# Optimization experiments

Hardware: AMD Instinct MI355X
Metric: run time of the kernel (lower is better)

Reference implementation:

```python
import jax, jax.numpy as jnp
import numpy as np

B, N = 8192, 2048


def setup_inputs() -> dict:
    key = jax.random.key(0)
    k1, k2 = jax.random.split(key)
    predictions = jax.random.normal(k1, (B, N), dtype=jnp.float32)
    targets = jax.random.normal(k2, (B, N), dtype=jnp.float32)
    return {"predictions": predictions, "targets": targets}


def reference(predictions, targets):
    # Original: per-batch NxN squared-difference cost matrix + scipy Hungarian,
    # then MSE(pred, optimally-permuted targets), averaged over the batch.
    # For scalar entries with cost (p_i - t_j)^2 the optimal assignment is the
    # monotone matching (rearrangement inequality): sort both vectors and pair
    # in order. This computes the exact same loss, fully vectorized.
    p_sorted = jnp.sort(predictions, axis=-1)  # [B, N]
    t_sorted = jnp.sort(targets, axis=-1)      # [B, N]
    # mean over N per row, then mean over B == global mean
    return jnp.mean((p_sorted - t_sorted) ** 2)
```

## Files before the change

### kernel.cpp

```cpp
#include <hip/hip_runtime.h>
#include <math.h>

#define ROWS 8192
#define NCOL 2048
#define V 32
#define WPB 4
#define THREADS (WPB * 64)

#define DPP_XOR1 0xB1
#define DPP_XOR2 0x4E
#define DPP_XOR3 0x1B
#define DPP_XOR7 0x141
#define DPP_XOR15 0x140

__device__ __forceinline__ void ce(float& a, float& b) {
  const float lo = fminf(a, b);
  const float hi = fmaxf(a, b);
  a = lo; b = hi;
}

__device__ __forceinline__ float ce_dir(float a, float b, float cdir) {
  return __builtin_amdgcn_fmed3f(a, b, cdir);
}

__device__ __forceinline__ float dirc(int lane, int bit) {
  return (lane & bit) ? INFINITY : -INFINITY;
}

template <int CTRL>
__device__ __forceinline__ float dpp_x(float x) {
  return __int_as_float(__builtin_amdgcn_update_dpp(
      0, __float_as_int(x), CTRL, 0xF, 0xF, true));
}

__device__ __forceinline__ float bperm(int addr, float x) {
  return __int_as_float(__builtin_amdgcn_ds_bpermute(addr, __float_as_int(x)));
}

template <int CTRL>
__device__ __forceinline__ void dpp_xor_pass(float r[V], float cdir) {
#pragma unroll
  for (int v = 0; v < V; ++v) r[v] = ce_dir(r[v], dpp_x<CTRL>(r[v]), cdir);
}

template <int CTRL>
__device__ __forceinline__ void dpp_flip_pass(float r[V], float cdir) {
#pragma unroll
  for (int q = 0; q < 8; ++q) {
    const int vA = 2 * q, vB = 2 * q + 1;
    float o[4];
    o[0] = dpp_x<CTRL>(r[vA ^ 31]);
    o[1] = dpp_x<CTRL>(r[vB ^ 31]);
    o[2] = dpp_x<CTRL>(r[vB]);
    o[3] = dpp_x<CTRL>(r[vA]);
    r[vA]      = ce_dir(r[vA],      o[0], cdir);
    r[vB]      = ce_dir(r[vB],      o[1], cdir);
    r[vB ^ 31] = ce_dir(r[vB ^ 31], o[2], cdir);
    r[vA ^ 31] = ce_dir(r[vA ^ 31], o[3], cdir);
  }
}

__device__ __forceinline__ void ds_xor_pass(float r[V], int addr, float cdir) {
#pragma unroll
  for (int c = 0; c < V; c += 8) {
    float o[8];
#pragma unroll
    for (int u = 0; u < 8; ++u) o[u] = bperm(addr, r[c + u]);
#pragma unroll
    for (int u = 0; u < 8; ++u) r[c + u] = ce_dir(r[c + u], o[u], cdir);
  }
}

__device__ __forceinline__ void ds_flip_pass(float r[V], int addr, float cdir) {
#pragma unroll
  for (int q = 0; q < 8; ++q) {
    const int vA = 2 * q, vB = 2 * q + 1;
    float o[4];
    o[0] = bperm(addr, r[vA ^ 31]);
    o[1] = bperm(addr, r[vB ^ 31]);
    o[2] = bperm(addr, r[vB]);
    o[3] = bperm(addr, r[vA]);
    r[vA]      = ce_dir(r[vA],      o[0], cdir);
    r[vB]      = ce_dir(r[vB],      o[1], cdir);
    r[vB ^ 31] = ce_dir(r[vB ^ 31], o[2], cdir);
    r[vA ^ 31] = ce_dir(r[vA ^ 31], o[3], cdir);
  }
}

__device__ __forceinline__ void inlane_tail(float rp[V], float rt[V]) {
#pragma unroll
  for (int j = 16; j >= 1; j >>= 1) {
#pragma unroll
    for (int v = 0; v < V; ++v) {
      if ((v & j) == 0) {
        ce(rp[v], rp[v | j]);
        ce(rt[v], rt[v | j]);
      }
    }
  }
}

__global__ __launch_bounds__(THREADS, 3) void sort_mse_kernel(
    const float* __restrict__ pred, const float* __restrict__ targ,
    float* __restrict__ out) {
  const int lane = threadIdx.x & 63;
  const int wave = threadIdx.x >> 6;
  const int row = blockIdx.x * WPB + wave;
  const size_t base = (size_t)row * NCOL + (size_t)lane * V;

  float rp[V], rt[V];
  const float4* p4 = (const float4*)(pred + base);
  const float4* t4 = (const float4*)(targ + base);
#pragma unroll
  for (int q = 0; q < V / 4; ++q) {
    const float4 a = p4[q];
    rp[4 * q + 0] = a.x; rp[4 * q + 1] = a.y;
    rp[4 * q + 2] = a.z; rp[4 * q + 3] = a.w;
    const float4 b = t4[q];
    rt[4 * q + 0] = b.x; rt[4 * q + 1] = b.y;
    rt[4 * q + 2] = b.z; rt[4 * q + 3] = b.w;
  }

#pragma unroll
  for (int k = 2; k <= V; k <<= 1) {
#pragma unroll
    for (int v = 0; v < V; ++v) {
      if ((v & (k >> 1)) == 0) {
        ce(rp[v], rp[v ^ (k - 1)]);
        ce(rt[v], rt[v ^ (k - 1)]);
      }
    }
#pragma unroll
    for (int j = k >> 2; j >= 1; j >>= 1) {
#pragma unroll
      for (int v = 0; v < V; ++v) {
        if ((v & j) == 0) {
          ce(rp[v], rp[v | j]);
          ce(rt[v], rt[v | j]);
        }
      }
    }
  }

#pragma unroll 1
  for (int kb = 1; kb <= 32; kb <<= 1) {
    const float cf = dirc(lane, kb);
    if (kb == 1) {
      dpp_flip_pass<DPP_XOR1>(rp, cf);  dpp_flip_pass<DPP_XOR1>(rt, cf);
    } else if (kb == 2) {
      dpp_flip_pass<DPP_XOR3>(rp, cf);  dpp_flip_pass<DPP_XOR3>(rt, cf);
    } else if (kb == 4) {
      dpp_flip_pass<DPP_XOR7>(rp, cf);  dpp_flip_pass<DPP_XOR7>(rt, cf);
    } else if (kb == 8) {
      dpp_flip_pass<DPP_XOR15>(rp, cf); dpp_flip_pass<DPP_XOR15>(rt, cf);
    } else {
      const int a = ((lane ^ (2 * kb - 1)) << 2);
      ds_flip_pass(rp, a, cf); ds_flip_pass(rt, a, cf);
    }
#pragma unroll 1
    for (int m = kb >> 1; m >= 1; m >>= 1) {
      const float c = dirc(lane, m);
      if (m == 1) {
        dpp_xor_pass<DPP_XOR1>(rp, c); dpp_xor_pass<DPP_XOR1>(rt, c);
      } else if (m == 2) {
        dpp_xor_pass<DPP_XOR2>(rp, c); dpp_xor_pass<DPP_XOR2>(rt, c);
      } else {
        const int a = ((lane ^ m) << 2);
        ds_xor_pass(rp, a, c); ds_xor_pass(rt, a, c);
      }
    }
    inlane_tail(rp, rt);
  }

  float acc = 0.f;
#pragma unroll
  for (int v = 0; v < V; ++v) {
    const float d = rp[v] - rt[v];
    acc = fmaf(d, d, acc);
  }
#pragma unroll
  for (int off = 32; off > 0; off >>= 1) acc += __shfl_down(acc, off, 64);
  if (lane == 0) {
    unsafeAtomicAdd(out, acc * (1.0f / ((float)ROWS * (float)NCOL)));
  }
}

extern "C" void kernel_launch(void* const* d_in, const int* in_sizes, int n_in,
                              void* d_out, int out_size, void* d_ws, size_t ws_size,
                              hipStream_t stream) {
  const float* pred = (const float*)d_in[0];
  const float* targ = (const float*)d_in[1];
  float* out = (float*)d_out;

  hipMemsetAsync(out, 0, sizeof(float), stream);
  sort_mse_kernel<<<ROWS / WPB, THREADS, 0, stream>>>(pred, targ, out);
}
```

Measured before the change: 248.7 us.

## Sort predictions and targets sequentially, stash sorted predictions in LDS, use DPP for xor4/xor8

Instead of sorting both rows together in registers, the kernel sorts the prediction row, parks it in swizzled shared memory, then sorts the target row and compares against the stash. This halves register pressure, so launch bounds go from 3 to 4 waves per SIMD. It also replaces the ds_bpermute exchanges for xor distances 4 and 8 with DPP shifts and row_xmask. The cost is lost ILP from no longer interleaving two independent sorts, plus an LDS round trip.

```diff
diff --git a/kernel.cpp b/kernel.cpp
--- a/kernel.cpp
+++ b/kernel.cpp
@@ -7,11 +7,14 @@
 #define WPB 4
 #define THREADS (WPB * 64)
 
-#define DPP_XOR1 0xB1
-#define DPP_XOR2 0x4E
-#define DPP_XOR3 0x1B
-#define DPP_XOR7 0x141
+#define DPP_XOR1  0xB1
+#define DPP_XOR2  0x4E
+#define DPP_XOR3  0x1B
+#define DPP_XOR7  0x141
 #define DPP_XOR15 0x140
+#define DPP_XOR8  0x128
+#define DPP_SHL4  0x104
+#define DPP_SHR4  0x114
 
 __device__ __forceinline__ void ce(float& a, float& b) {
   const float lo = fminf(a, b);
@@ -41,6 +44,16 @@
 __device__ __forceinline__ void dpp_xor_pass(float r[V], float cdir) {
 #pragma unroll
   for (int v = 0; v < V; ++v) r[v] = ce_dir(r[v], dpp_x<CTRL>(r[v]), cdir);
+}
+
+__device__ __forceinline__ void dpp_xor4_pass(float r[V], float cdir, int lane) {
+  const bool hi = (lane & 4) != 0;
+#pragma unroll
+  for (int v = 0; v < V; ++v) {
+    const float a = dpp_x<DPP_SHL4>(r[v]);
+    const float b = dpp_x<DPP_SHR4>(r[v]);
+    r[v] = ce_dir(r[v], hi ? b : a, cdir);
+  }
 }
 
 template <int CTRL>
@@ -87,96 +100,85 @@
   }
 }
 
-__device__ __forceinline__ void inlane_tail(float rp[V], float rt[V]) {
+__device__ __forceinline__ void sort_row(float r[V], const int lane) {
 #pragma unroll
-  for (int j = 16; j >= 1; j >>= 1) {
+  for (int k = 2; k <= V; k <<= 1) {
 #pragma unroll
-    for (int v = 0; v < V; ++v) {
-      if ((v & j) == 0) {
-        ce(rp[v], rp[v | j]);
-        ce(rt[v], rt[v | j]);
-      }
+    for (int v = 0; v < V; ++v)
+      if ((v & (k >> 1)) == 0) ce(r[v], r[v ^ (k - 1)]);
+#pragma unroll
+    for (int j = k >> 2; j >= 1; j >>= 1)
+#pragma unroll
+      for (int v = 0; v < V; ++v)
+        if ((v & j) == 0) ce(r[v], r[v | j]);
+  }
+#pragma unroll 1
+  for (int kb = 1; kb <= 32; kb <<= 1) {
+    const float cf = dirc(lane, kb);
+    if (kb == 1)      dpp_flip_pass<DPP_XOR1>(r, cf);
+    else if (kb == 2) dpp_flip_pass<DPP_XOR3>(r, cf);
+    else if (kb == 4) dpp_flip_pass<DPP_XOR7>(r, cf);
+    else if (kb == 8) dpp_flip_pass<DPP_XOR15>(r, cf);
+    else ds_flip_pass(r, (lane ^ (2 * kb - 1)) << 2, cf);
+#pragma unroll 1
+    for (int m = kb >> 1; m >= 1; m >>= 1) {
+      const float c = dirc(lane, m);
+      if (m == 1)      dpp_xor_pass<DPP_XOR1>(r, c);
+      else if (m == 2) dpp_xor_pass<DPP_XOR2>(r, c);
+      else if (m == 4) dpp_xor4_pass(r, c, lane);
+      else if (m == 8) dpp_xor_pass<DPP_XOR8>(r, c);
+      else ds_xor_pass(r, (lane ^ m) << 2, c);
     }
+#pragma unroll
+    for (int j = 16; j >= 1; j >>= 1)
+#pragma unroll
+      for (int v = 0; v < V; ++v)
+        if ((v & j) == 0) ce(r[v], r[v | j]);
   }
 }
 
-__global__ __launch_bounds__(THREADS, 3) void sort_mse_kernel(
+__global__ __launch_bounds__(THREADS, 4) void sort_mse_kernel(
     const float* __restrict__ pred, const float* __restrict__ targ,
     float* __restrict__ out) {
+  __shared__ float4 stash[WPB * 512];
   const int lane = threadIdx.x & 63;
   const int wave = threadIdx.x >> 6;
   const int row = blockIdx.x * WPB + wave;
   const size_t base = (size_t)row * NCOL + (size_t)lane * V;
+  float4* ws = &stash[wave * 512 + lane * 8];
 
-  float rp[V], rt[V];
+  float r[V];
   const float4* p4 = (const float4*)(pred + base);
+#pragma unroll
+  for (int q = 0; q < 8; ++q) {
+    const float4 a = p4[q];
+    r[4 * q + 0] = a.x; r[4 * q + 1] = a.y;
+    r[4 * q + 2] = a.z; r[4 * q + 3] = a.w;
+  }
+  sort_row(r, lane);
+#pragma unroll
+  for (int q = 0; q < 8; ++q)
+    ws[q ^ (lane & 7)] =
+        make_float4(r[4 * q + 0], r[4 * q + 1], r[4 * q + 2], r[4 * q + 3]);
+
   const float4* t4 = (const float4*)(targ + base);
 #pragma unroll
-  for (int q = 0; q < V / 4; ++q) {
-    const float4 a = p4[q];
-    rp[4 * q + 0] = a.x; rp[4 * q + 1] = a.y;
-    rp[4 * q + 2] = a.z; rp[4 * q + 3] = a.w;
-    const float4 b = t4[q];
-    rt[4 * q + 0] = b.x; rt[4 * q + 1] = b.y;
-    rt[4 * q + 2] = b.z; rt[4 * q + 3] = b.w;
+  for (int q = 0; q < 8; ++q) {
+    const float4 a = t4[q];
+    r[4 * q + 0] = a.x; r[4 * q + 1] = a.y;
+    r[4 * q + 2] = a.z; r[4 * q + 3] = a.w;
   }
-
-#pragma unroll
-  for (int k = 2; k <= V; k <<= 1) {
-#pragma unroll
-    for (int v = 0; v < V; ++v) {
-      if ((v & (k >> 1)) == 0) {
-        ce(rp[v], rp[v ^ (k - 1)]);
-        ce(rt[v], rt[v ^ (k - 1)]);
-      }
-    }
-#pragma unroll
-    for (int j = k >> 2; j >= 1; j >>= 1) {
-#pragma unroll
-      for (int v = 0; v < V; ++v) {
-        if ((v & j) == 0) {
-          ce(rp[v], rp[v | j]);
-          ce(rt[v], rt[v | j]);
-        }
-      }
-    }
-  }
-
-#pragma unroll 1
-  for (int kb = 1; kb <= 32; kb <<= 1) {
-    const float cf = dirc(lane, kb);
-    if (kb == 1) {
-      dpp_flip_pass<DPP_XOR1>(rp, cf);  dpp_flip_pass<DPP_XOR1>(rt, cf);
-    } else if (kb == 2) {
-      dpp_flip_pass<DPP_XOR3>(rp, cf);  dpp_flip_pass<DPP_XOR3>(rt, cf);
-    } else if (kb == 4) {
-      dpp_flip_pass<DPP_XOR7>(rp, cf);  dpp_flip_pass<DPP_XOR7>(rt, cf);
-    } else if (kb == 8) {
-      dpp_flip_pass<DPP_XOR15>(rp, cf); dpp_flip_pass<DPP_XOR15>(rt, cf);
-    } else {
-      const int a = ((lane ^ (2 * kb - 1)) << 2);
-      ds_flip_pass(rp, a, cf); ds_flip_pass(rt, a, cf);
-    }
-#pragma unroll 1
-    for (int m = kb >> 1; m >= 1; m >>= 1) {
-      const float c = dirc(lane, m);
-      if (m == 1) {
-        dpp_xor_pass<DPP_XOR1>(rp, c); dpp_xor_pass<DPP_XOR1>(rt, c);
-      } else if (m == 2) {
-        dpp_xor_pass<DPP_XOR2>(rp, c); dpp_xor_pass<DPP_XOR2>(rt, c);
-      } else {
-        const int a = ((lane ^ m) << 2);
-        ds_xor_pass(rp, a, c); ds_xor_pass(rt, a, c);
-      }
-    }
-    inlane_tail(rp, rt);
-  }
+  sort_row(r, lane);
 
   float acc = 0.f;
 #pragma unroll
-  for (int v = 0; v < V; ++v) {
-    const float d = rp[v] - rt[v];
-    acc = fmaf(d, d, acc);
+  for (int q = 0; q < 8; ++q) {
+    const float4 s = ws[q ^ (lane & 7)];
+    float d;
+    d = s.x - r[4 * q + 0]; acc = fmaf(d, d, acc);
+    d = s.y - r[4 * q + 1]; acc = fmaf(d, d, acc);
+    d = s.z - r[4 * q + 2]; acc = fmaf(d, d, acc);
+    d = s.w - r[4 * q + 3]; acc = fmaf(d, d, acc);
   }
 #pragma unroll
   for (int off = 32; off > 0; off >>= 1) acc += __shfl_down(acc, off, 64);
```

Result: no change. 250.9 us (+0.9%).
